# Performance work log

Measured on AMD Instinct MI355X. Metric: run time of the kernel, lower is better.

Reference implementation:

```python
import jax, jax.numpy as jnp
import numpy as np

N = 4096
D = 256
H = 8
E = 131072
NEG = -1e30  # stands in for -inf; keeps grads NaN-free


def setup_inputs() -> dict:
    key = jax.random.key(0)
    ks = jax.random.split(key, 8)
    s = 1.0 / np.sqrt(D)
    return {
        "x": jax.random.normal(ks[0], (N, D), dtype=jnp.float32),
        "edge_index": jax.random.randint(ks[1], (2, E), 0, N, dtype=jnp.int32),
        "Wq": jax.random.normal(ks[2], (D, D), dtype=jnp.float32) * s,
        "Wk": jax.random.normal(ks[3], (D, D), dtype=jnp.float32) * s,
        "Wv": jax.random.normal(ks[4], (D, D), dtype=jnp.float32) * s,
        "Wo": jax.random.normal(ks[5], (D, D), dtype=jnp.float32) * s,
        "bo": jnp.zeros((D,), dtype=jnp.float32),
        "gamma": jnp.ones((D,), dtype=jnp.float32),
        "beta": jnp.zeros((D,), dtype=jnp.float32),
    }


def reference(x, edge_index, Wq, Wk, Wv, Wo, bo, gamma, beta):
    n, d_model = x.shape
    d_h = d_model // H
    scale = jnp.sqrt(jnp.float32(d_h))

    # mask: True = blocked. Diagonal and graph edges (dst attends to src) unblocked.
    mask = jnp.ones((n, n), dtype=bool)
    diag = jnp.arange(n)
    mask = mask.at[diag, diag].set(False)
    src, dst = edge_index[0], edge_index[1]
    mask = mask.at[dst, src].set(False)

    # projections: torch Linear computes x @ W.T
    Q = (x @ Wq.T).reshape(n, H, d_h).transpose(1, 0, 2)  # [H, N, d_h]
    K = (x @ Wk.T).reshape(n, H, d_h).transpose(1, 0, 2)
    V = (x @ Wv.T).reshape(n, H, d_h).transpose(1, 0, 2)

    scores = jnp.einsum("hnd,hmd->hnm", Q, K) / scale      # [H, N, N]
    scores = jnp.where(mask[None, :, :], NEG, scores)
    attn = jax.nn.softmax(scores, axis=-1)
    attn = jnp.nan_to_num(attn, nan=0.0)

    out = jnp.einsum("hnm,hmd->hnd", attn, V)              # [H, N, d_h]
    out = out.transpose(1, 0, 2).reshape(n, d_model)
    out = out @ Wo.T + bo

    # LayerNorm(x + out), eps=1e-5
    h = x + out
    mu = jnp.mean(h, axis=-1, keepdims=True)
    var = jnp.var(h, axis=-1, keepdims=True)
    return (h - mu) * jax.lax.rsqrt(var + 1e-5) * gamma + beta
```

## Files before the change

### kernel.cpp

```cpp
#include <hip/hip_runtime.h>

#define D_MODEL 256
#define N_HEADS 8
#define MAXN 128
#define NGEMM 384

typedef __attribute__((ext_vector_type(8))) short bf16x8;
typedef __attribute__((ext_vector_type(4))) float f32x4;

__device__ __forceinline__ unsigned short f2bf(float f) {
    union { float f; unsigned int u; } v; v.f = f;
    unsigned int r = v.u + 0x7fff + ((v.u >> 16) & 1);
    return (unsigned short)(r >> 16);
}
__device__ __forceinline__ float bf2f(unsigned short u) {
    union { unsigned int u; float f; } v; v.u = ((unsigned int)u) << 16;
    return v.f;
}

__global__ void prep_kernel(const float* __restrict__ x,
                            const float* __restrict__ W0, const float* __restrict__ W1,
                            const float* __restrict__ W2, const float* __restrict__ W3,
                            unsigned short* __restrict__ xb,
                            unsigned short* __restrict__ O0, unsigned short* __restrict__ O1,
                            unsigned short* __restrict__ O2, unsigned short* __restrict__ O3,
                            unsigned long long* __restrict__ mask, int n) {
    const int XV = (4096 * 256) / 4;
    int i = blockIdx.x * blockDim.x + threadIdx.x;

    int wpr = n >> 6;
    int mwords = n * wpr;
    if (i < mwords) {
        int row = i >> 6;
        int w = i & 63;
        mask[i] = (w == (row >> 6)) ? (1ULL << (row & 63)) : 0ULL;
    }

    const float* src;
    unsigned short* dst;
    int k;
    if (i < XV) {
        src = x; dst = xb; k = i;
    } else {
        int i2 = i - XV;
        if (i2 >= 4 * 16384) return;
        int z = i2 >> 14;
        k = i2 & 16383;
        src = (z == 0) ? W0 : (z == 1) ? W1 : (z == 2) ? W2 : W3;
        dst = (z == 0) ? O0 : (z == 1) ? O1 : (z == 2) ? O2 : O3;
    }
    float4 v = *(const float4*)(src + (size_t)k * 4);
    ushort4 o;
    o.x = f2bf(v.x); o.y = f2bf(v.y); o.z = f2bf(v.z); o.w = f2bf(v.w);
    *(ushort4*)(dst + (size_t)k * 4) = o;
}

__global__ __launch_bounds__(256) void qkv_edges_kernel(
        const unsigned short* __restrict__ xb,
        const unsigned short* __restrict__ Wq, const unsigned short* __restrict__ Wk,
        const unsigned short* __restrict__ Wv,
        unsigned short* __restrict__ Qb, unsigned short* __restrict__ Kb,
        unsigned short* __restrict__ Vb,
        const int* __restrict__ ei, unsigned long long* __restrict__ mask,
        int E, int n) {
    int blk = blockIdx.x;
    if (blk >= NGEMM) {
        int e = (blk - NGEMM) * 256 + threadIdx.x;
        if (e < E) {
            int src = ei[e];
            int dst = ei[E + e];
            int wpr = n >> 6;
            atomicOr(&mask[(size_t)dst * wpr + (src >> 6)], 1ULL << (src & 63));
        }
        return;
    }
    int z = blk >> 7;
    int r = blk & 127;
    int by = r >> 2, bx = r & 3;
    const unsigned short* B = (z == 0) ? Wq : (z == 1) ? Wk : Wv;
    unsigned short* Cb = (z == 0) ? Qb : (z == 1) ? Kb : Vb;

    __shared__ short Alds[128][72];
    __shared__ short Blds[64][72];
    int t = threadIdx.x;
    int wave = t >> 6, lane = t & 63;
    int wr = wave >> 1, wc = wave & 1;
    int lr = t >> 3;
    int lk = (t & 7) << 3;

    const unsigned short* Abase = xb + ((size_t)(by * 128 + lr)) * D_MODEL + lk;
    const unsigned short* Bbase = B + ((size_t)(bx * 64 + lr)) * D_MODEL + lk;

    int fm = lane & 15;
    int fk = (lane >> 4) << 3;

    f32x4 acc[4][2];
#pragma unroll
    for (int rr = 0; rr < 4; ++rr)
#pragma unroll
        for (int c = 0; c < 2; ++c) acc[rr][c] = (f32x4){0.f, 0.f, 0.f, 0.f};

    for (int k0 = 0; k0 < D_MODEL; k0 += 64) {
        *(uint4*)&Alds[lr][lk]      = *(const uint4*)(Abase + k0);
        *(uint4*)&Alds[lr + 32][lk] = *(const uint4*)(Abase + 32 * D_MODEL + k0);
        *(uint4*)&Alds[lr + 64][lk] = *(const uint4*)(Abase + 64 * D_MODEL + k0);
        *(uint4*)&Alds[lr + 96][lk] = *(const uint4*)(Abase + 96 * D_MODEL + k0);
        *(uint4*)&Blds[lr][lk]      = *(const uint4*)(Bbase + k0);
        *(uint4*)&Blds[lr + 32][lk] = *(const uint4*)(Bbase + 32 * D_MODEL + k0);
        __syncthreads();
#pragma unroll
        for (int ks = 0; ks < 64; ks += 32) {
            bf16x8 af[4], bf[2];
#pragma unroll
            for (int rr = 0; rr < 4; ++rr)
                af[rr] = *(const bf16x8*)&Alds[wr * 64 + rr * 16 + fm][ks + fk];
#pragma unroll
            for (int c = 0; c < 2; ++c)
                bf[c] = *(const bf16x8*)&Blds[wc * 32 + c * 16 + fm][ks + fk];
#pragma unroll
            for (int rr = 0; rr < 4; ++rr)
#pragma unroll
                for (int c = 0; c < 2; ++c)
                    acc[rr][c] = __builtin_amdgcn_mfma_f32_16x16x32_bf16(
                        af[rr], bf[c], acc[rr][c], 0, 0, 0);
        }
        __syncthreads();
    }

    int orow0 = by * 128 + wr * 64 + ((lane >> 4) << 2);
    int ocol0 = bx * 64 + wc * 32 + (lane & 15);
#pragma unroll
    for (int rr = 0; rr < 4; ++rr)
#pragma unroll
        for (int c = 0; c < 2; ++c)
#pragma unroll
            for (int q = 0; q < 4; ++q)
                Cb[(size_t)(orow0 + rr * 16 + q) * D_MODEL + ocol0 + c * 16] =
                    f2bf(acc[rr][c][q]);
}

__global__ __launch_bounds__(64) void attn_kernel(
        const unsigned short* __restrict__ Qb, const unsigned short* __restrict__ Kb,
        const unsigned short* __restrict__ Vb,
        const unsigned long long* __restrict__ mask,
        unsigned short* __restrict__ Ob, int n) {
    int dst = blockIdx.x;
    int L = threadIdx.x;
    int wpr = n >> 6;

    __shared__ int nbr[MAXN + 16];
    __shared__ float s_lds[N_HEADS][MAXN];

    unsigned long long w = (L < wpr) ? mask[(size_t)dst * wpr + L] : 0ULL;
    int c = __popcll(w);
    int xs = c;
#pragma unroll
    for (int o = 1; o < 64; o <<= 1) {
        int y = __shfl_up(xs, o, 64);
        if (L >= o) xs += y;
    }
    int pos = xs - c;
    while (w) {
        int b = __builtin_ctzll(w);
        w &= w - 1;
        if (pos < MAXN) nbr[pos] = (L << 6) + b;
        ++pos;
    }
    int cnt = __shfl(xs, 63, 64);
    if (cnt > MAXN) cnt = MAXN;
    int nb = (cnt + 15) & ~15;
    __syncthreads();
    int last = nbr[cnt - 1];
    if (L < nb - cnt) nbr[cnt + L] = last;
    __syncthreads();

    int col = L & 15;
    int kq = L >> 4;
    bf16x8 qf = (bf16x8){0, 0, 0, 0, 0, 0, 0, 0};
    if (col < N_HEADS)
        qf = *(const bf16x8*)(Qb + (size_t)dst * D_MODEL + col * 32 + kq * 8);
    const bf16x8 zf = (bf16x8){0, 0, 0, 0, 0, 0, 0, 0};
    const float inv_scale = 0.17677669529663687f;

    for (int b0 = 0; b0 < nb; b0 += 16) {
        int nj = nbr[b0 + col];
        const unsigned short* krow = Kb + (size_t)nj * D_MODEL + kq * 8;
        f32x4 c0 = (f32x4){0.f, 0.f, 0.f, 0.f};
        f32x4 c1 = (f32x4){0.f, 0.f, 0.f, 0.f};
#pragma unroll
        for (int kb = 0; kb < 8; kb += 2) {
            bf16x8 a0 = *(const bf16x8*)(krow + kb * 32);
            bf16x8 a1 = *(const bf16x8*)(krow + kb * 32 + 32);
            bf16x8 bop0 = (col == kb)     ? qf : zf;
            bf16x8 bop1 = (col == kb + 1) ? qf : zf;
            c0 = __builtin_amdgcn_mfma_f32_16x16x32_bf16(a0, bop0, c0, 0, 0, 0);
            c1 = __builtin_amdgcn_mfma_f32_16x16x32_bf16(a1, bop1, c1, 0, 0, 0);
        }
        if (col < N_HEADS) {
            int jr = b0 + kq * 4;
            float4 o4;
            float s0 = (c0[0] + c1[0]) * inv_scale;
            float s1 = (c0[1] + c1[1]) * inv_scale;
            float s2 = (c0[2] + c1[2]) * inv_scale;
            float s3 = (c0[3] + c1[3]) * inv_scale;
            o4.x = (jr + 0 < cnt) ? s0 : -1e30f;
            o4.y = (jr + 1 < cnt) ? s1 : -1e30f;
            o4.z = (jr + 2 < cnt) ? s2 : -1e30f;
            o4.w = (jr + 3 < cnt) ? s3 : -1e30f;
            *(float4*)&s_lds[col][jr] = o4;
        }
    }
    __syncthreads();

    int h = L >> 3, li = L & 7;
    float m = -1e30f;
    for (int j0 = li * 4; j0 < nb; j0 += 32) {
        float4 v = *(const float4*)&s_lds[h][j0];
        m = fmaxf(m, fmaxf(fmaxf(v.x, v.y), fmaxf(v.z, v.w)));
    }
    m = fmaxf(m, __shfl_xor(m, 1, 8));
    m = fmaxf(m, __shfl_xor(m, 2, 8));
    m = fmaxf(m, __shfl_xor(m, 4, 8));
    float l = 0.f;
    for (int j0 = li * 4; j0 < nb; j0 += 32) {
        float4 v = *(const float4*)&s_lds[h][j0];
        float4 e4;
        e4.x = __expf(v.x - m); e4.y = __expf(v.y - m);
        e4.z = __expf(v.z - m); e4.w = __expf(v.w - m);
        *(float4*)&s_lds[h][j0] = e4;
        l += (e4.x + e4.y) + (e4.z + e4.w);
    }
    l += __shfl_xor(l, 1, 8);
    l += __shfl_xor(l, 2, 8);
    l += __shfl_xor(l, 4, 8);
    __syncthreads();

    f32x4 acc = (f32x4){0.f, 0.f, 0.f, 0.f};
    const unsigned short* vb = Vb + 4 * L;
    for (int j = 0; j < nb; j += 4) {
        float4 wv = *(const float4*)&s_lds[h][j];
        int j0 = nbr[j], j1 = nbr[j + 1], j2 = nbr[j + 2], j3 = nbr[j + 3];
        uint2 r0 = *(const uint2*)(vb + (size_t)j0 * D_MODEL);
        uint2 r1 = *(const uint2*)(vb + (size_t)j1 * D_MODEL);
        uint2 r2 = *(const uint2*)(vb + (size_t)j2 * D_MODEL);
        uint2 r3 = *(const uint2*)(vb + (size_t)j3 * D_MODEL);
        acc[0] += wv.x * bf2f((unsigned short)(r0.x & 0xffff));
        acc[1] += wv.x * bf2f((unsigned short)(r0.x >> 16));
        acc[2] += wv.x * bf2f((unsigned short)(r0.y & 0xffff));
        acc[3] += wv.x * bf2f((unsigned short)(r0.y >> 16));
        acc[0] += wv.y * bf2f((unsigned short)(r1.x & 0xffff));
        acc[1] += wv.y * bf2f((unsigned short)(r1.x >> 16));
        acc[2] += wv.y * bf2f((unsigned short)(r1.y & 0xffff));
        acc[3] += wv.y * bf2f((unsigned short)(r1.y >> 16));
        acc[0] += wv.z * bf2f((unsigned short)(r2.x & 0xffff));
        acc[1] += wv.z * bf2f((unsigned short)(r2.x >> 16));
        acc[2] += wv.z * bf2f((unsigned short)(r2.y & 0xffff));
        acc[3] += wv.z * bf2f((unsigned short)(r2.y >> 16));
        acc[0] += wv.w * bf2f((unsigned short)(r3.x & 0xffff));
        acc[1] += wv.w * bf2f((unsigned short)(r3.x >> 16));
        acc[2] += wv.w * bf2f((unsigned short)(r3.y & 0xffff));
        acc[3] += wv.w * bf2f((unsigned short)(r3.y >> 16));
    }
    float rl = 1.f / l;
    ushort4 o;
    o.x = f2bf(acc[0] * rl); o.y = f2bf(acc[1] * rl);
    o.z = f2bf(acc[2] * rl); o.w = f2bf(acc[3] * rl);
    *(ushort4*)(Ob + (size_t)dst * D_MODEL + 4 * L) = o;
}

struct SMemO {
    union {
        struct { short A[32][72]; short B[256][72]; } st;
        float c[32][260];
    };
};

__global__ __launch_bounds__(256) void gemm_o_ln_kernel(
        const unsigned short* __restrict__ Ob, const unsigned short* __restrict__ Wob,
        const float* __restrict__ x, const float* __restrict__ bo,
        const float* __restrict__ gamma, const float* __restrict__ beta,
        float* __restrict__ out) {
    __shared__ SMemO sm;
    int by = blockIdx.x;
    int t = threadIdx.x;
    int wave = t >> 6, lane = t & 63;
    int rt = wave >> 1, cq = wave & 1;
    int lr = t >> 3;
    int lk = (t & 7) << 3;

    const unsigned short* Abase = Ob + ((size_t)(by * 32 + lr)) * D_MODEL + lk;
    int fm = lane & 15;
    int fk = (lane >> 4) << 3;

    f32x4 acc[8];
#pragma unroll
    for (int ct = 0; ct < 8; ++ct) acc[ct] = (f32x4){0.f, 0.f, 0.f, 0.f};

    for (int k0 = 0; k0 < D_MODEL; k0 += 64) {
        *(uint4*)&sm.st.A[lr][lk] = *(const uint4*)(Abase + k0);
#pragma unroll
        for (int j = 0; j < 8; ++j)
            *(uint4*)&sm.st.B[lr + 32 * j][lk] =
                *(const uint4*)(Wob + ((size_t)(lr + 32 * j)) * D_MODEL + k0 + lk);
        __syncthreads();
#pragma unroll
        for (int ks = 0; ks < 64; ks += 32) {
            bf16x8 af = *(const bf16x8*)&sm.st.A[rt * 16 + fm][ks + fk];
#pragma unroll
            for (int ct = 0; ct < 8; ++ct) {
                bf16x8 bf = *(const bf16x8*)&sm.st.B[cq * 128 + ct * 16 + fm][ks + fk];
                acc[ct] = __builtin_amdgcn_mfma_f32_16x16x32_bf16(af, bf, acc[ct], 0, 0, 0);
            }
        }
        __syncthreads();
    }

    int rr0 = rt * 16 + ((lane >> 4) << 2);
#pragma unroll
    for (int ct = 0; ct < 8; ++ct)
#pragma unroll
        for (int q = 0; q < 4; ++q)
            sm.c[rr0 + q][cq * 128 + ct * 16 + (lane & 15)] = acc[ct][q];
    __syncthreads();

    float4 bo4 = *(const float4*)(bo + lane * 4);
    float4 g4  = *(const float4*)(gamma + lane * 4);
    float4 be4 = *(const float4*)(beta + lane * 4);
#pragma unroll
    for (int rr = 0; rr < 8; ++rr) {
        int r = wave * 8 + rr;
        int grow = by * 32 + r;
        float4 p = *(const float4*)&sm.c[r][lane * 4];
        float4 xv = *(const float4*)(x + (size_t)grow * D_MODEL + lane * 4);
        float hx = p.x + xv.x + bo4.x;
        float hy = p.y + xv.y + bo4.y;
        float hz = p.z + xv.z + bo4.z;
        float hw = p.w + xv.w + bo4.w;
        float s  = (hx + hy) + (hz + hw);
        float s2 = (hx * hx + hy * hy) + (hz * hz + hw * hw);
#pragma unroll
        for (int o = 32; o; o >>= 1) {
            s  += __shfl_xor(s, o, 64);
            s2 += __shfl_xor(s2, o, 64);
        }
        float mu = s * (1.f / 256.f);
        float var = s2 * (1.f / 256.f) - mu * mu;
        float rstd = rsqrtf(var + 1e-5f);
        float4 o4;
        o4.x = (hx - mu) * rstd * g4.x + be4.x;
        o4.y = (hy - mu) * rstd * g4.y + be4.y;
        o4.z = (hz - mu) * rstd * g4.z + be4.z;
        o4.w = (hw - mu) * rstd * g4.w + be4.w;
        *(float4*)(out + (size_t)grow * D_MODEL + lane * 4) = o4;
    }
}

extern "C" void kernel_launch(void* const* d_in, const int* in_sizes, int n_in,
                              void* d_out, int out_size, void* d_ws, size_t ws_size,
                              hipStream_t stream) {
    const float* x     = (const float*)d_in[0];
    const int*   ei    = (const int*)  d_in[1];
    const float* Wq    = (const float*)d_in[2];
    const float* Wk    = (const float*)d_in[3];
    const float* Wv    = (const float*)d_in[4];
    const float* Wo    = (const float*)d_in[5];
    const float* bo    = (const float*)d_in[6];
    const float* gamma = (const float*)d_in[7];
    const float* beta  = (const float*)d_in[8];
    float* out = (float*)d_out;

    int n = in_sizes[0] / D_MODEL;
    int E = in_sizes[1] / 2;

    char* ws = (char*)d_ws;
    size_t off = 0;
    unsigned long long* mask = (unsigned long long*)(ws + off);
    off += (size_t)n * (n >> 6) * sizeof(unsigned long long);
    unsigned short* xb  = (unsigned short*)(ws + off); off += (size_t)n * D_MODEL * 2;
    unsigned short* Wqb = (unsigned short*)(ws + off); off += D_MODEL * D_MODEL * 2;
    unsigned short* Wkb = (unsigned short*)(ws + off); off += D_MODEL * D_MODEL * 2;
    unsigned short* Wvb = (unsigned short*)(ws + off); off += D_MODEL * D_MODEL * 2;
    unsigned short* Wob = (unsigned short*)(ws + off); off += D_MODEL * D_MODEL * 2;
    unsigned short* Qb  = (unsigned short*)(ws + off); off += (size_t)n * D_MODEL * 2;
    unsigned short* Kb  = (unsigned short*)(ws + off); off += (size_t)n * D_MODEL * 2;
    unsigned short* Vb  = (unsigned short*)(ws + off); off += (size_t)n * D_MODEL * 2;
    unsigned short* Ob  = (unsigned short*)(ws + off); off += (size_t)n * D_MODEL * 2;

    prep_kernel<<<1280, 256, 0, stream>>>(x, Wq, Wk, Wv, Wo,
                                          xb, Wqb, Wkb, Wvb, Wob, mask, n);

    int edge_blocks = (E + 255) / 256;
    qkv_edges_kernel<<<NGEMM + edge_blocks, 256, 0, stream>>>(
        xb, Wqb, Wkb, Wvb, Qb, Kb, Vb, ei, mask, E, n);

    attn_kernel<<<n, 64, 0, stream>>>(Qb, Kb, Vb, mask, Ob, n);

    gemm_o_ln_kernel<<<n / 32, 256, 0, stream>>>(Ob, Wob, x, bo, gamma, beta, out);
}
```

Baseline: 113.1 us.

## Fuse attention into single-pass online softmax with double-buffered K prefetch

Replaces the three-phase attention (scores written to LDS, then max/exp passes, then PV accumulation) with one loop over 16-neighbor tiles using an online softmax. Per-tile max and sum are reduced through cross-lane shuffles, and exp weights are broadcast by shuffle instead of going through shared memory. The next tile's K rows are loaded into a second register buffer while the current tile is processed, and V gathers are issued early to hide latency. The cost is more registers, rescaling exps on every tile, and many shuffles, which may reduce occupancy.

```diff
diff --git a/kernel.cpp b/kernel.cpp
--- a/kernel.cpp
+++ b/kernel.cpp
@@ -139,6 +139,130 @@
                     f2bf(acc[rr][c][q]);
 }
 
+#define LOAD_K(KR, tt)                                                        \
+    do {                                                                      \
+        int _ti = (tt);                                                       \
+        if (_ti < nt) {                                                       \
+            int _ix = nbr[_ti * 16 + col];                                    \
+            const unsigned short* _kr = Kb + _ix * D_MODEL + (kq << 3);       \
+            KR[0] = *(const bf16x8*)(_kr + 0 * 32);                           \
+            KR[1] = *(const bf16x8*)(_kr + 1 * 32);                           \
+            KR[2] = *(const bf16x8*)(_kr + 2 * 32);                           \
+            KR[3] = *(const bf16x8*)(_kr + 3 * 32);                           \
+            KR[4] = *(const bf16x8*)(_kr + 4 * 32);                           \
+            KR[5] = *(const bf16x8*)(_kr + 5 * 32);                           \
+            KR[6] = *(const bf16x8*)(_kr + 6 * 32);                           \
+            KR[7] = *(const bf16x8*)(_kr + 7 * 32);                           \
+        }                                                                     \
+    } while (0)
+
+#define FMA4(P, W, V)                                                         \
+    do {                                                                      \
+        P[0] += (W) * bf2f((unsigned short)((V).x & 0xffff));                 \
+        P[1] += (W) * bf2f((unsigned short)((V).x >> 16));                    \
+        P[2] += (W) * bf2f((unsigned short)((V).y & 0xffff));                 \
+        P[3] += (W) * bf2f((unsigned short)((V).y >> 16));                    \
+    } while (0)
+
+#define TILE_BODY(KC, KN, tt)                                                 \
+    do {                                                                      \
+        int _t = (tt);                                                        \
+        int _b0 = _t << 4;                                                    \
+                                 \
+        int4 _i0 = *(const int4*)&nbr[_b0];                                   \
+        int4 _i1 = *(const int4*)&nbr[_b0 + 4];                               \
+        int4 _i2 = *(const int4*)&nbr[_b0 + 8];                               \
+        int4 _i3 = *(const int4*)&nbr[_b0 + 12];                              \
+          \
+        uint2 _v0  = *(const uint2*)(vbase + _i0.x * D_MODEL);                \
+        uint2 _v1  = *(const uint2*)(vbase + _i0.y * D_MODEL);                \
+        uint2 _v2  = *(const uint2*)(vbase + _i0.z * D_MODEL);                \
+        uint2 _v3  = *(const uint2*)(vbase + _i0.w * D_MODEL);                \
+        uint2 _v4  = *(const uint2*)(vbase + _i1.x * D_MODEL);                \
+        uint2 _v5  = *(const uint2*)(vbase + _i1.y * D_MODEL);                \
+        uint2 _v6  = *(const uint2*)(vbase + _i1.z * D_MODEL);                \
+        uint2 _v7  = *(const uint2*)(vbase + _i1.w * D_MODEL);                \
+        uint2 _v8  = *(const uint2*)(vbase + _i2.x * D_MODEL);                \
+        uint2 _v9  = *(const uint2*)(vbase + _i2.y * D_MODEL);                \
+        uint2 _v10 = *(const uint2*)(vbase + _i2.z * D_MODEL);                \
+        uint2 _v11 = *(const uint2*)(vbase + _i2.w * D_MODEL);                \
+        uint2 _v12 = *(const uint2*)(vbase + _i3.x * D_MODEL);                \
+        uint2 _v13 = *(const uint2*)(vbase + _i3.y * D_MODEL);                \
+        uint2 _v14 = *(const uint2*)(vbase + _i3.z * D_MODEL);                \
+        uint2 _v15 = *(const uint2*)(vbase + _i3.w * D_MODEL);                \
+                          \
+        LOAD_K(KN, _t + 1);                                                   \
+                 \
+        f32x4 _c0 = (f32x4){0.f, 0.f, 0.f, 0.f};                              \
+        f32x4 _c1 = (f32x4){0.f, 0.f, 0.f, 0.f};                              \
+        _c0 = __builtin_amdgcn_mfma_f32_16x16x32_bf16(KC[0], (col == 0) ? qf : zf, _c0, 0, 0, 0); \
+        _c1 = __builtin_amdgcn_mfma_f32_16x16x32_bf16(KC[1], (col == 1) ? qf : zf, _c1, 0, 0, 0); \
+        _c0 = __builtin_amdgcn_mfma_f32_16x16x32_bf16(KC[2], (col == 2) ? qf : zf, _c0, 0, 0, 0); \
+        _c1 = __builtin_amdgcn_mfma_f32_16x16x32_bf16(KC[3], (col == 3) ? qf : zf, _c1, 0, 0, 0); \
+        _c0 = __builtin_amdgcn_mfma_f32_16x16x32_bf16(KC[4], (col == 4) ? qf : zf, _c0, 0, 0, 0); \
+        _c1 = __builtin_amdgcn_mfma_f32_16x16x32_bf16(KC[5], (col == 5) ? qf : zf, _c1, 0, 0, 0); \
+        _c0 = __builtin_amdgcn_mfma_f32_16x16x32_bf16(KC[6], (col == 6) ? qf : zf, _c0, 0, 0, 0); \
+        _c1 = __builtin_amdgcn_mfma_f32_16x16x32_bf16(KC[7], (col == 7) ? qf : zf, _c1, 0, 0, 0); \
+        float _s0 = (_c0[0] + _c1[0]) * inv_scale;                            \
+        float _s1 = (_c0[1] + _c1[1]) * inv_scale;                            \
+        float _s2 = (_c0[2] + _c1[2]) * inv_scale;                            \
+        float _s3 = (_c0[3] + _c1[3]) * inv_scale;                            \
+        int _jr = _b0 + (kq << 2);                                            \
+        _s0 = (_jr + 0 < cnt) ? _s0 : -1e30f;                                 \
+        _s1 = (_jr + 1 < cnt) ? _s1 : -1e30f;                                 \
+        _s2 = (_jr + 2 < cnt) ? _s2 : -1e30f;                                 \
+        _s3 = (_jr + 3 < cnt) ? _s3 : -1e30f;                                 \
+        \
+        float _mt = fmaxf(fmaxf(_s0, _s1), fmaxf(_s2, _s3));                  \
+        _mt = fmaxf(_mt, __shfl_xor(_mt, 16, 64));                            \
+        _mt = fmaxf(_mt, __shfl_xor(_mt, 32, 64));                            \
+        float _w0 = __expf(_s0 - _mt);                                        \
+        float _w1 = __expf(_s1 - _mt);                                        \
+        float _w2 = __expf(_s2 - _mt);                                        \
+        float _w3 = __expf(_s3 - _mt);                                        \
+        float _ts = (_w0 + _w1) + (_w2 + _w3);                                \
+        _ts += __shfl_xor(_ts, 16, 64);                                       \
+        _ts += __shfl_xor(_ts, 32, 64);                                       \
+                       \
+        float _mh = __shfl(_mt, h, 64);                                       \
+        float _th = __shfl(_ts, h, 64);                                       \
+        float _mn = fmaxf(m, _mh);                                            \
+        float _so = __expf(m - _mn);                                          \
+        float _f  = __expf(_mh - _mn);                                        \
+        m = _mn;                                                              \
+        l = l * _so + _th * _f;                                               \
+             \
+        f32x4 _p = (f32x4){0.f, 0.f, 0.f, 0.f};                               \
+        {                                                                     \
+            float _wa = __shfl(_w0, h, 64), _wb = __shfl(_w1, h, 64);         \
+            float _wc = __shfl(_w2, h, 64), _wd = __shfl(_w3, h, 64);         \
+            FMA4(_p, _wa, _v0); FMA4(_p, _wb, _v1);                           \
+            FMA4(_p, _wc, _v2); FMA4(_p, _wd, _v3);                           \
+        }                                                                     \
+        {                                                                     \
+            float _wa = __shfl(_w0, h + 16, 64), _wb = __shfl(_w1, h + 16, 64); \
+            float _wc = __shfl(_w2, h + 16, 64), _wd = __shfl(_w3, h + 16, 64); \
+            FMA4(_p, _wa, _v4); FMA4(_p, _wb, _v5);                           \
+            FMA4(_p, _wc, _v6); FMA4(_p, _wd, _v7);                           \
+        }                                                                     \
+        {                                                                     \
+            float _wa = __shfl(_w0, h + 32, 64), _wb = __shfl(_w1, h + 32, 64); \
+            float _wc = __shfl(_w2, h + 32, 64), _wd = __shfl(_w3, h + 32, 64); \
+            FMA4(_p, _wa, _v8); FMA4(_p, _wb, _v9);                           \
+            FMA4(_p, _wc, _v10); FMA4(_p, _wd, _v11);                         \
+        }                                                                     \
+        {                                                                     \
+            float _wa = __shfl(_w0, h + 48, 64), _wb = __shfl(_w1, h + 48, 64); \
+            float _wc = __shfl(_w2, h + 48, 64), _wd = __shfl(_w3, h + 48, 64); \
+            FMA4(_p, _wa, _v12); FMA4(_p, _wb, _v13);                         \
+            FMA4(_p, _wc, _v14); FMA4(_p, _wd, _v15);                         \
+        }                                                                     \
+        acc[0] = acc[0] * _so + _p[0] * _f;                                   \
+        acc[1] = acc[1] * _so + _p[1] * _f;                                   \
+        acc[2] = acc[2] * _so + _p[2] * _f;                                   \
+        acc[3] = acc[3] * _so + _p[3] * _f;                                   \
+    } while (0)
+
 __global__ __launch_bounds__(64) void attn_kernel(
         const unsigned short* __restrict__ Qb, const unsigned short* __restrict__ Kb,
         const unsigned short* __restrict__ Vb,
@@ -148,8 +272,7 @@
     int L = threadIdx.x;
     int wpr = n >> 6;
 
-    __shared__ int nbr[MAXN + 16];
-    __shared__ float s_lds[N_HEADS][MAXN];
+    __shared__ alignas(16) int nbr[MAXN + 16];
 
     unsigned long long w = (L < wpr) ? mask[(size_t)dst * wpr + L] : 0ULL;
     int c = __popcll(w);
@@ -173,6 +296,7 @@
     int last = nbr[cnt - 1];
     if (L < nb - cnt) nbr[cnt + L] = last;
     __syncthreads();
+    int nt = nb >> 4;
 
     int col = L & 15;
     int kq = L >> 4;
@@ -182,85 +306,19 @@
     const bf16x8 zf = (bf16x8){0, 0, 0, 0, 0, 0, 0, 0};
     const float inv_scale = 0.17677669529663687f;
 
-    for (int b0 = 0; b0 < nb; b0 += 16) {
-        int nj = nbr[b0 + col];
-        const unsigned short* krow = Kb + (size_t)nj * D_MODEL + kq * 8;
-        f32x4 c0 = (f32x4){0.f, 0.f, 0.f, 0.f};
-        f32x4 c1 = (f32x4){0.f, 0.f, 0.f, 0.f};
-#pragma unroll
-        for (int kb = 0; kb < 8; kb += 2) {
-            bf16x8 a0 = *(const bf16x8*)(krow + kb * 32);
-            bf16x8 a1 = *(const bf16x8*)(krow + kb * 32 + 32);
-            bf16x8 bop0 = (col == kb)     ? qf : zf;
-            bf16x8 bop1 = (col == kb + 1) ? qf : zf;
-            c0 = __builtin_amdgcn_mfma_f32_16x16x32_bf16(a0, bop0, c0, 0, 0, 0);
-            c1 = __builtin_amdgcn_mfma_f32_16x16x32_bf16(a1, bop1, c1, 0, 0, 0);
-        }
-        if (col < N_HEADS) {
-            int jr = b0 + kq * 4;
-            float4 o4;
-            float s0 = (c0[0] + c1[0]) * inv_scale;
-            float s1 = (c0[1] + c1[1]) * inv_scale;
-            float s2 = (c0[2] + c1[2]) * inv_scale;
-            float s3 = (c0[3] + c1[3]) * inv_scale;
-            o4.x = (jr + 0 < cnt) ? s0 : -1e30f;
-            o4.y = (jr + 1 < cnt) ? s1 : -1e30f;
-            o4.z = (jr + 2 < cnt) ? s2 : -1e30f;
-            o4.w = (jr + 3 < cnt) ? s3 : -1e30f;
-            *(float4*)&s_lds[col][jr] = o4;
-        }
-    }
-    __syncthreads();
-
-    int h = L >> 3, li = L & 7;
-    float m = -1e30f;
-    for (int j0 = li * 4; j0 < nb; j0 += 32) {
-        float4 v = *(const float4*)&s_lds[h][j0];
-        m = fmaxf(m, fmaxf(fmaxf(v.x, v.y), fmaxf(v.z, v.w)));
-    }
-    m = fmaxf(m, __shfl_xor(m, 1, 8));
-    m = fmaxf(m, __shfl_xor(m, 2, 8));
-    m = fmaxf(m, __shfl_xor(m, 4, 8));
-    float l = 0.f;
-    for (int j0 = li * 4; j0 < nb; j0 += 32) {
-        float4 v = *(const float4*)&s_lds[h][j0];
-        float4 e4;
-        e4.x = __expf(v.x - m); e4.y = __expf(v.y - m);
-        e4.z = __expf(v.z - m); e4.w = __expf(v.w - m);
-        *(float4*)&s_lds[h][j0] = e4;
-        l += (e4.x + e4.y) + (e4.z + e4.w);
-    }
-    l += __shfl_xor(l, 1, 8);
-    l += __shfl_xor(l, 2, 8);
-    l += __shfl_xor(l, 4, 8);
-    __syncthreads();
-
+    int h = L >> 3;
+    const unsigned short* vbase = Vb + 4 * L;
+
+    float m = -1e30f, l = 0.f;
     f32x4 acc = (f32x4){0.f, 0.f, 0.f, 0.f};
-    const unsigned short* vb = Vb + 4 * L;
-    for (int j = 0; j < nb; j += 4) {
-        float4 wv = *(const float4*)&s_lds[h][j];
-        int j0 = nbr[j], j1 = nbr[j + 1], j2 = nbr[j + 2], j3 = nbr[j + 3];
-        uint2 r0 = *(const uint2*)(vb + (size_t)j0 * D_MODEL);
-        uint2 r1 = *(const uint2*)(vb + (size_t)j1 * D_MODEL);
-        uint2 r2 = *(const uint2*)(vb + (size_t)j2 * D_MODEL);
-        uint2 r3 = *(const uint2*)(vb + (size_t)j3 * D_MODEL);
-        acc[0] += wv.x * bf2f((unsigned short)(r0.x & 0xffff));
-        acc[1] += wv.x * bf2f((unsigned short)(r0.x >> 16));
-        acc[2] += wv.x * bf2f((unsigned short)(r0.y & 0xffff));
-        acc[3] += wv.x * bf2f((unsigned short)(r0.y >> 16));
-        acc[0] += wv.y * bf2f((unsigned short)(r1.x & 0xffff));
-        acc[1] += wv.y * bf2f((unsigned short)(r1.x >> 16));
-        acc[2] += wv.y * bf2f((unsigned short)(r1.y & 0xffff));
-        acc[3] += wv.y * bf2f((unsigned short)(r1.y >> 16));
-        acc[0] += wv.z * bf2f((unsigned short)(r2.x & 0xffff));
-        acc[1] += wv.z * bf2f((unsigned short)(r2.x >> 16));
-        acc[2] += wv.z * bf2f((unsigned short)(r2.y & 0xffff));
-        acc[3] += wv.z * bf2f((unsigned short)(r2.y >> 16));
-        acc[0] += wv.w * bf2f((unsigned short)(r3.x & 0xffff));
-        acc[1] += wv.w * bf2f((unsigned short)(r3.x >> 16));
-        acc[2] += wv.w * bf2f((unsigned short)(r3.y & 0xffff));
-        acc[3] += wv.w * bf2f((unsigned short)(r3.y >> 16));
-    }
+
+    bf16x8 KA[8], KBx[8];
+    LOAD_K(KA, 0);
+    for (int t = 0; t < nt; t += 2) {
+        TILE_BODY(KA, KBx, t);
+        if (t + 1 < nt) TILE_BODY(KBx, KA, t + 1);
+    }
+
     float rl = 1.f / l;
     ushort4 o;
     o.x = f2bf(acc[0] * rl); o.y = f2bf(acc[1] * rl);
```

Result: slower. 115.8 us (+2.3%).

## Fuse fp32-to-bf16 conversion into QKV GEMM loads and drop prep kernel

Applied to the files above, without the earlier changes.

Removes the separate prep kernel that converted x and all weights to bf16 and initialised the mask. The QKV GEMM now reads fp32 x and weights directly and converts them while staging into LDS. The Wo conversion moves into extra blocks of the same launch, and the mask is zeroed with a memset, with the diagonal bit added inside the attention kernel. This removes a launch and a round trip of bf16 copies through memory. In exchange the GEMM reads twice the bytes per tile and repeats the conversion work across blocks that share tiles.

```diff
diff --git a/kernel.cpp b/kernel.cpp
--- a/kernel.cpp
+++ b/kernel.cpp
@@ -4,6 +4,7 @@
 #define N_HEADS 8
 #define MAXN 128
 #define NGEMM 384
+#define NCONV 16
 
 typedef __attribute__((ext_vector_type(8))) short bf16x8;
 typedef __attribute__((ext_vector_type(4))) float f32x4;
@@ -17,55 +18,33 @@
     union { unsigned int u; float f; } v; v.u = ((unsigned int)u) << 16;
     return v.f;
 }
-
-__global__ void prep_kernel(const float* __restrict__ x,
-                            const float* __restrict__ W0, const float* __restrict__ W1,
-                            const float* __restrict__ W2, const float* __restrict__ W3,
-                            unsigned short* __restrict__ xb,
-                            unsigned short* __restrict__ O0, unsigned short* __restrict__ O1,
-                            unsigned short* __restrict__ O2, unsigned short* __restrict__ O3,
-                            unsigned long long* __restrict__ mask, int n) {
-    const int XV = (4096 * 256) / 4;
-    int i = blockIdx.x * blockDim.x + threadIdx.x;
-
-    int wpr = n >> 6;
-    int mwords = n * wpr;
-    if (i < mwords) {
-        int row = i >> 6;
-        int w = i & 63;
-        mask[i] = (w == (row >> 6)) ? (1ULL << (row & 63)) : 0ULL;
-    }
-
-    const float* src;
-    unsigned short* dst;
-    int k;
-    if (i < XV) {
-        src = x; dst = xb; k = i;
-    } else {
-        int i2 = i - XV;
-        if (i2 >= 4 * 16384) return;
-        int z = i2 >> 14;
-        k = i2 & 16383;
-        src = (z == 0) ? W0 : (z == 1) ? W1 : (z == 2) ? W2 : W3;
-        dst = (z == 0) ? O0 : (z == 1) ? O1 : (z == 2) ? O2 : O3;
-    }
-    float4 v = *(const float4*)(src + (size_t)k * 4);
+__device__ __forceinline__ ushort4 cvt4(float4 v) {
     ushort4 o;
     o.x = f2bf(v.x); o.y = f2bf(v.y); o.z = f2bf(v.z); o.w = f2bf(v.w);
-    *(ushort4*)(dst + (size_t)k * 4) = o;
+    return o;
 }
 
 __global__ __launch_bounds__(256) void qkv_edges_kernel(
-        const unsigned short* __restrict__ xb,
-        const unsigned short* __restrict__ Wq, const unsigned short* __restrict__ Wk,
-        const unsigned short* __restrict__ Wv,
+        const float* __restrict__ x,
+        const float* __restrict__ Wq, const float* __restrict__ Wk,
+        const float* __restrict__ Wv, const float* __restrict__ Wo,
         unsigned short* __restrict__ Qb, unsigned short* __restrict__ Kb,
-        unsigned short* __restrict__ Vb,
+        unsigned short* __restrict__ Vb, unsigned short* __restrict__ Wob,
         const int* __restrict__ ei, unsigned long long* __restrict__ mask,
         int E, int n) {
     int blk = blockIdx.x;
     if (blk >= NGEMM) {
-        int e = (blk - NGEMM) * 256 + threadIdx.x;
+        int b2 = blk - NGEMM;
+        if (b2 < NCONV) {
+            int i = (b2 * 256 + threadIdx.x) * 16;
+            const float* s = Wo + i;
+            unsigned short* d = Wob + i;
+#pragma unroll
+            for (int j = 0; j < 4; ++j)
+                *(ushort4*)(d + 4 * j) = cvt4(*(const float4*)(s + 4 * j));
+            return;
+        }
+        int e = (b2 - NCONV) * 256 + threadIdx.x;
         if (e < E) {
             int src = ei[e];
             int dst = ei[E + e];
@@ -77,7 +56,7 @@
     int z = blk >> 7;
     int r = blk & 127;
     int by = r >> 2, bx = r & 3;
-    const unsigned short* B = (z == 0) ? Wq : (z == 1) ? Wk : Wv;
+    const float* B = (z == 0) ? Wq : (z == 1) ? Wk : Wv;
     unsigned short* Cb = (z == 0) ? Qb : (z == 1) ? Kb : Vb;
 
     __shared__ short Alds[128][72];
@@ -88,8 +67,8 @@
     int lr = t >> 3;
     int lk = (t & 7) << 3;
 
-    const unsigned short* Abase = xb + ((size_t)(by * 128 + lr)) * D_MODEL + lk;
-    const unsigned short* Bbase = B + ((size_t)(bx * 64 + lr)) * D_MODEL + lk;
+    const float* Abase = x + ((size_t)(by * 128 + lr)) * D_MODEL + lk;
+    const float* Bbase = B + ((size_t)(bx * 64 + lr)) * D_MODEL + lk;
 
     int fm = lane & 15;
     int fk = (lane >> 4) << 3;
@@ -101,12 +80,20 @@
         for (int c = 0; c < 2; ++c) acc[rr][c] = (f32x4){0.f, 0.f, 0.f, 0.f};
 
     for (int k0 = 0; k0 < D_MODEL; k0 += 64) {
-        *(uint4*)&Alds[lr][lk]      = *(const uint4*)(Abase + k0);
-        *(uint4*)&Alds[lr + 32][lk] = *(const uint4*)(Abase + 32 * D_MODEL + k0);
-        *(uint4*)&Alds[lr + 64][lk] = *(const uint4*)(Abase + 64 * D_MODEL + k0);
-        *(uint4*)&Alds[lr + 96][lk] = *(const uint4*)(Abase + 96 * D_MODEL + k0);
-        *(uint4*)&Blds[lr][lk]      = *(const uint4*)(Bbase + k0);
-        *(uint4*)&Blds[lr + 32][lk] = *(const uint4*)(Bbase + 32 * D_MODEL + k0);
+#pragma unroll
+        for (int j = 0; j < 4; ++j) {
+            float4 va = *(const float4*)(Abase + (size_t)j * 32 * D_MODEL + k0);
+            float4 vb = *(const float4*)(Abase + (size_t)j * 32 * D_MODEL + k0 + 4);
+            *(ushort4*)&Alds[lr + 32 * j][lk]     = cvt4(va);
+            *(ushort4*)&Alds[lr + 32 * j][lk + 4] = cvt4(vb);
+        }
+#pragma unroll
+        for (int j = 0; j < 2; ++j) {
+            float4 va = *(const float4*)(Bbase + (size_t)j * 32 * D_MODEL + k0);
+            float4 vb = *(const float4*)(Bbase + (size_t)j * 32 * D_MODEL + k0 + 4);
+            *(ushort4*)&Blds[lr + 32 * j][lk]     = cvt4(va);
+            *(ushort4*)&Blds[lr + 32 * j][lk + 4] = cvt4(vb);
+        }
         __syncthreads();
 #pragma unroll
         for (int ks = 0; ks < 64; ks += 32) {
@@ -152,6 +139,7 @@
     __shared__ float s_lds[N_HEADS][MAXN];
 
     unsigned long long w = (L < wpr) ? mask[(size_t)dst * wpr + L] : 0ULL;
+    if (L == (dst >> 6)) w |= 1ULL << (dst & 63);
     int c = __popcll(w);
     int xs = c;
 #pragma unroll
@@ -375,23 +363,19 @@
     char* ws = (char*)d_ws;
     size_t off = 0;
     unsigned long long* mask = (unsigned long long*)(ws + off);
-    off += (size_t)n * (n >> 6) * sizeof(unsigned long long);
-    unsigned short* xb  = (unsigned short*)(ws + off); off += (size_t)n * D_MODEL * 2;
-    unsigned short* Wqb = (unsigned short*)(ws + off); off += D_MODEL * D_MODEL * 2;
-    unsigned short* Wkb = (unsigned short*)(ws + off); off += D_MODEL * D_MODEL * 2;
-    unsigned short* Wvb = (unsigned short*)(ws + off); off += D_MODEL * D_MODEL * 2;
+    size_t mask_bytes = (size_t)n * (n >> 6) * sizeof(unsigned long long);
+    off += mask_bytes;
     unsigned short* Wob = (unsigned short*)(ws + off); off += D_MODEL * D_MODEL * 2;
     unsigned short* Qb  = (unsigned short*)(ws + off); off += (size_t)n * D_MODEL * 2;
     unsigned short* Kb  = (unsigned short*)(ws + off); off += (size_t)n * D_MODEL * 2;
     unsigned short* Vb  = (unsigned short*)(ws + off); off += (size_t)n * D_MODEL * 2;
     unsigned short* Ob  = (unsigned short*)(ws + off); off += (size_t)n * D_MODEL * 2;
 
-    prep_kernel<<<1280, 256, 0, stream>>>(x, Wq, Wk, Wv, Wo,
-                                          xb, Wqb, Wkb, Wvb, Wob, mask, n);
+    hipMemsetAsync(mask, 0, mask_bytes, stream);
 
     int edge_blocks = (E + 255) / 256;
-    qkv_edges_kernel<<<NGEMM + edge_blocks, 256, 0, stream>>>(
-        xb, Wqb, Wkb, Wvb, Qb, Kb, Vb, ei, mask, E, n);
+    qkv_edges_kernel<<<NGEMM + NCONV + edge_blocks, 256, 0, stream>>>(
+        x, Wq, Wk, Wv, Wo, Qb, Kb, Vb, Wob, ei, mask, E, n);
 
     attn_kernel<<<n, 64, 0, stream>>>(Qb, Kb, Vb, mask, Ob, n);
 
```

After: 113.9 us, median of 2. About the same (+0.7%).
